# Kernel tuning notes

Hardware: AMD Instinct MI355X
Metric: run time of the kernel (lower is better)

Reference implementation:

```python
import jax, jax.numpy as jnp
import numpy as np

N_NODES = 100000
N_EDGES = 3200000
N_GRAPHS = 256
VOCAB = 1500


def gcn_conv(x, edge_index, W, b, n_nodes):
    # x: [N, Fin], edge_index: [2, E] (row=source, col=target)
    h = x @ W  # [N, Fout]
    loops = jnp.arange(n_nodes, dtype=edge_index.dtype)
    row = jnp.concatenate([edge_index[0], loops])
    col = jnp.concatenate([edge_index[1], loops])
    # symmetric normalization with self-loops (PyG GCNConv default)
    deg = jax.ops.segment_sum(jnp.ones_like(col, dtype=h.dtype), col,
                              num_segments=n_nodes)
    dinv = jnp.where(deg > 0, jax.lax.rsqrt(deg), 0.0)
    norm = dinv[row] * dinv[col]  # [E+N]
    msg = h[row] * norm[:, None]  # gather + scale
    out = jax.ops.segment_sum(msg, col, num_segments=n_nodes)  # scatter-add
    return out + b


def setup_inputs() -> dict:
    key = jax.random.key(0)
    k = jax.random.split(key, 8)
    x_ids = jax.random.randint(k[0], (N_NODES,), 0, VOCAB)
    edge_index = jax.random.randint(k[1], (2, N_EDGES), 0, N_NODES)
    batch = jnp.sort(jax.random.randint(k[2], (N_NODES,), 0, N_GRAPHS))
    emb_table = jax.random.normal(k[3], (VOCAB, 16), dtype=jnp.float32)
    W1 = jax.random.normal(k[4], (16, 32), dtype=jnp.float32) * (1.0 / np.sqrt(16))
    b1 = jnp.zeros((32,), dtype=jnp.float32)
    W2 = jax.random.normal(k[5], (32, 41), dtype=jnp.float32) * (1.0 / np.sqrt(32))
    b2 = jnp.zeros((41,), dtype=jnp.float32)
    return {"x_ids": x_ids, "edge_index": edge_index, "batch": batch,
            "emb_table": emb_table, "W1": W1, "b1": b1, "W2": W2, "b2": b2}


def reference(x_ids, edge_index, batch, emb_table, W1, b1, W2, b2):
    x = emb_table[x_ids]                      # embedding lookup [N,16]
    x = gcn_conv(x, edge_index, W1, b1, N_NODES)
    x = jax.nn.relu(x)                        # dropout is identity in eval
    x = gcn_conv(x, edge_index, W2, b2, N_NODES)
    # scatter_add pooling over graphs in batch
    return jax.ops.segment_sum(x, batch, num_segments=N_GRAPHS)  # [G,41]
```

## Files before the change

### kernel.cpp

```cpp
#include <hip/hip_runtime.h>


constexpr int EPB = 16384;
constexpr int BSH = 8;
constexpr int BKTN = 1 << BSH;
constexpr int CAP = 10240;
constexpr int CAPC = 8704;

__device__ inline unsigned short f2bf(float x) {
  unsigned u = __float_as_uint(x);
  u += 0x7FFF + ((u >> 16) & 1);
  return (unsigned short)(u >> 16);
}
__device__ inline float bf2f(unsigned short h) {
  return __uint_as_float((unsigned)h << 16);
}
__device__ inline unsigned pk(float a, float b) {
  return (unsigned)f2bf(a) | ((unsigned)f2bf(b) << 16);
}
__device__ __forceinline__ void add8(float acc[8], uint4 v) {
  acc[0] += bf2f(v.x & 0xFFFF); acc[1] += bf2f(v.x >> 16);
  acc[2] += bf2f(v.y & 0xFFFF); acc[3] += bf2f(v.y >> 16);
  acc[4] += bf2f(v.z & 0xFFFF); acc[5] += bf2f(v.z >> 16);
  acc[6] += bf2f(v.w & 0xFFFF); acc[7] += bf2f(v.w >> 16);
}

__device__ __forceinline__ void gather8(const unsigned short* __restrict__ base,
                                        const int* list, int st, int dg,
                                        float acc[8]) {
  int j = 0;
  if (dg >= 8) {
    int r0 = list[st], r1 = list[st + 1], r2 = list[st + 2], r3 = list[st + 3];
    uint4 v0 = *(const uint4*)(base + (size_t)r0 * 16);
    uint4 v1 = *(const uint4*)(base + (size_t)r1 * 16);
    uint4 v2 = *(const uint4*)(base + (size_t)r2 * 16);
    uint4 v3 = *(const uint4*)(base + (size_t)r3 * 16);
    for (j = 4; j + 4 <= dg; j += 4) {
      int s0 = list[st + j], s1 = list[st + j + 1];
      int s2 = list[st + j + 2], s3 = list[st + j + 3];
      uint4 w0 = *(const uint4*)(base + (size_t)s0 * 16);
      uint4 w1 = *(const uint4*)(base + (size_t)s1 * 16);
      uint4 w2 = *(const uint4*)(base + (size_t)s2 * 16);
      uint4 w3 = *(const uint4*)(base + (size_t)s3 * 16);
      add8(acc, v0); add8(acc, v1); add8(acc, v2); add8(acc, v3);
      v0 = w0; v1 = w1; v2 = w2; v3 = w3;
    }
    add8(acc, v0); add8(acc, v1); add8(acc, v2); add8(acc, v3);
  }
  for (; j < dg; ++j)
    add8(acc, *(const uint4*)(base + (size_t)list[st + j] * 16));
}

__device__ __forceinline__ void copy_window(int* list, const int* __restrict__ src,
                                            int n, int tid) {
  const int4* s4 = (const int4*)src;
  int4* d4 = (int4*)list;
  int n4 = n >> 2;
  for (int i = tid; i < n4; i += 512) d4[i] = s4[i];
  for (int i = (n4 << 2) + tid; i < n; i += 512) list[i] = src[i];
}

__device__ __forceinline__ int swz(int b, int nblkp) {
  return (b & 7) * (nblkp >> 3) + (b >> 3);
}

__global__ __launch_bounds__(1024) void k_scatter(const int* __restrict__ row,
                                                  const int* __restrict__ col, int E,
                                                  int nbkt, int nblkp,
                                                  int* __restrict__ cursor,
                                                  int* __restrict__ staging) {
  __shared__ int sbuf[EPB];
  __shared__ int cnt[512], sc[512], cur[512], gbase[512];
  int tid = threadIdx.x;
  int lane = tid & 63, wv = tid >> 6;
  int blk = swz(blockIdx.x, nblkp);
  if (tid < 512) cnt[tid] = 0;
  __syncthreads();
  int e0 = blk * EPB, e1 = min(E, e0 + EPB);
  for (int e = e0 + tid; e < e1; e += 1024)
    atomicAdd(&cnt[col[e] >> BSH], 1);
  __syncthreads();
  if (tid < 512) {
    int c = cnt[tid];
    sc[tid] = c;
    gbase[tid] = c ? atomicAdd(&cursor[tid], c) : 0;
  }
  __syncthreads();
  for (int o = 1; o < 512; o <<= 1) {
    int u = (tid < 512 && tid >= o) ? sc[tid - o] : 0;
    __syncthreads();
    if (tid < 512) sc[tid] += u;
    __syncthreads();
  }
  if (tid < 512) { int st = sc[tid] - cnt[tid]; sc[tid] = st; cur[tid] = st; }
  __syncthreads();
  for (int e = e0 + tid; e < e1; e += 1024) {
    int c = col[e];
    int b = c >> BSH;
    int pos = atomicAdd(&cur[b], 1);
    sbuf[pos] = (row[e] << BSH) | (c & (BKTN - 1));
  }
  __syncthreads();
  for (int b = wv; b < nbkt; b += 16) {
    int lbeg = sc[b], lcnt = cnt[b];
    int gb = gbase[b];
    int lim = CAP - gb;
    if (lcnt > lim) lcnt = lim > 0 ? lim : 0;
    int g = b * CAP + gb;
    for (int j = lane; j < lcnt; j += 64)
      staging[g + j] = sbuf[lbeg + j];
  }
}

__global__ __launch_bounds__(512) void k_build(const int* __restrict__ staging,
                                               const int* __restrict__ cursor,
                                               const int* __restrict__ x_ids,
                                               const float* __restrict__ emb,
                                               int N, int nbkt,
                                               int* __restrict__ col_ptr,
                                               int* __restrict__ endp,
                                               float* __restrict__ dinv,
                                               unsigned short* __restrict__ ag1,
                                               int* __restrict__ edge_row) {
  __shared__ int list[CAP];
  __shared__ int cnt[BKTN], sc[BKTN], lcur[BKTN];
  int tid = threadIdx.x, b = blockIdx.x;
  int beg = b * CAP;
  int total = min(cursor[b], CAP);
  int end = beg + total;
  if (tid < BKTN) cnt[tid] = 0;
  __syncthreads();
  for (int i = beg + tid; i < end; i += 512)
    atomicAdd(&cnt[staging[i] & (BKTN - 1)], 1);
  __syncthreads();
  if (tid < BKTN) sc[tid] = cnt[tid];
  __syncthreads();
  for (int o = 1; o < BKTN; o <<= 1) {
    int u = (tid < BKTN && tid >= o) ? sc[tid - o] : 0;
    __syncthreads();
    if (tid < BKTN) sc[tid] += u;
    __syncthreads();
  }
  if (tid < BKTN) {
    int excl = sc[tid] - cnt[tid];
    sc[tid] = excl;
    lcur[tid] = excl;
    int node = (b << BSH) + tid;
    if (node < N) col_ptr[node] = beg + excl;
  }
  if (tid == 0) {
    endp[b] = end;
    if (b == nbkt - 1) col_ptr[N] = end;
  }
  __syncthreads();
  for (int i = beg + tid; i < end; i += 512) {
    int p = staging[i];
    list[atomicAdd(&lcur[p & (BKTN - 1)], 1)] = p >> BSH;
  }
  __syncthreads();
  for (int i = beg + tid; i < end; i += 512)
    edge_row[i] = list[i - beg];
  int nloc = tid >> 1, half = tid & 1;
  int node = (b << BSH) + nloc;
  if (node < N) {
    float d = rsqrtf((float)(cnt[nloc] + 1));
    if (half == 0) dinv[node] = d;
    const float* er = emb + (size_t)x_ids[node] * 16 + half * 8;
    float4 e0 = *(const float4*)(er);
    float4 e1 = *(const float4*)(er + 4);
    uint4 o;
    o.x = pk(e0.x * d, e0.y * d); o.y = pk(e0.z * d, e0.w * d);
    o.z = pk(e1.x * d, e1.y * d); o.w = pk(e1.z * d, e1.w * d);
    *(uint4*)(ag1 + (size_t)node * 16 + half * 8) = o;
  }
}

__global__ __launch_bounds__(512) void k_fuse1(const unsigned short* __restrict__ ag1,
                                               const int* __restrict__ edge_row,
                                               const int* __restrict__ col_ptr,
                                               const int* __restrict__ endp,
                                               const float* __restrict__ dinv,
                                               const float* __restrict__ W1,
                                               const float* __restrict__ b1, int N,
                                               unsigned short* __restrict__ y1g) {
  __shared__ int list[CAPC];
  __shared__ float W[512];
  __shared__ float bb[32];
  int tid = threadIdx.x, b = blockIdx.x;
  W[tid] = W1[tid];
  if (tid < 32) bb[tid] = b1[tid];
  int nloc = tid >> 1, half = tid & 1;
  int node = (b << BSH) + nloc;
  bool valid = node < N;
  int beg = b * CAP;
  int end = endp[b];
  int ms = 0, me = 0;
  float acc[8];
  if (valid) {
    ms = col_ptr[node];
    me = (nloc == BKTN - 1) ? end : col_ptr[node + 1];
    uint4 v = *(const uint4*)(ag1 + (size_t)node * 16 + half * 8);
    acc[0] = bf2f(v.x & 0xFFFF); acc[1] = bf2f(v.x >> 16);
    acc[2] = bf2f(v.y & 0xFFFF); acc[3] = bf2f(v.y >> 16);
    acc[4] = bf2f(v.z & 0xFFFF); acc[5] = bf2f(v.z >> 16);
    acc[6] = bf2f(v.w & 0xFFFF); acc[7] = bf2f(v.w >> 16);
  } else {
#pragma unroll
    for (int k = 0; k < 8; ++k) acc[k] = 0.f;
  }
  for (int cbeg = beg; cbeg < end; cbeg += CAPC) {
    int cend = min(end, cbeg + CAPC);
    __syncthreads();
    copy_window(list, edge_row + cbeg, cend - cbeg, tid);
    __syncthreads();
    if (valid) {
      int st = max(ms, cbeg), en = min(me, cend);
      if (en > st) gather8(ag1 + half * 8, list, st - cbeg, en - st, acc);
    }
  }
  if (!valid) return;
  float d = dinv[node];
  float sx[8], xo[8];
#pragma unroll
  for (int k = 0; k < 8; ++k) sx[k] = acc[k] * d;
#pragma unroll
  for (int k = 0; k < 8; ++k) xo[k] = __shfl_xor(sx[k], 1);
  float x[16];
  if (half == 0) {
#pragma unroll
    for (int k = 0; k < 8; ++k) { x[k] = sx[k]; x[8 + k] = xo[k]; }
  } else {
#pragma unroll
    for (int k = 0; k < 8; ++k) { x[k] = xo[k]; x[8 + k] = sx[k]; }
  }
  int j0 = half * 16;
  float a[16];
#pragma unroll
  for (int j = 0; j < 16; ++j) a[j] = bb[j0 + j];
#pragma unroll
  for (int k = 0; k < 16; ++k) {
    float xv = x[k];
#pragma unroll
    for (int j = 0; j < 16; ++j) a[j] += xv * W[k * 32 + j0 + j];
  }
#pragma unroll
  for (int j = 0; j < 16; ++j) a[j] = fmaxf(a[j], 0.f) * d;
  uint4 o0 = {pk(a[0], a[1]), pk(a[2], a[3]), pk(a[4], a[5]), pk(a[6], a[7])};
  uint4 o1 = {pk(a[8], a[9]), pk(a[10], a[11]), pk(a[12], a[13]), pk(a[14], a[15])};
  unsigned short* yp = y1g + (size_t)half * N * 16 + (size_t)node * 16;
  *(uint4*)(yp) = o0;
  *(uint4*)(yp + 8) = o1;
}

__global__ __launch_bounds__(512) void k_fuse2(const unsigned short* __restrict__ y1g,
                                               const int* __restrict__ edge_row,
                                               const int* __restrict__ col_ptr,
                                               const int* __restrict__ endp,
                                               const float* __restrict__ dinv,
                                               const int* __restrict__ batch, int N,
                                               int nbkt, float* __restrict__ P) {
  __shared__ int list[CAPC];
  __shared__ float pool[8 * 16];
  int bx = blockIdx.x;
  int plane = (bx >> 2) & 1;
  int b = (bx >> 3) * 4 + (bx & 3);
  if (b >= nbkt) return;
  const unsigned short* __restrict__ y1p = y1g + (size_t)plane * N * 16;
  int pofs = plane << 4;
  int tid = threadIdx.x;
  int nloc = tid >> 1, half = tid & 1;
  int node = (b << BSH) + nloc;
  bool valid = node < N;
  int beg = b * CAP;
  int end = endp[b];
  int ms = 0, me = 0;
  float acc[8];
  if (valid) {
    ms = col_ptr[node];
    me = (nloc == BKTN - 1) ? end : col_ptr[node + 1];
    uint4 v = *(const uint4*)(y1p + (size_t)node * 16 + half * 8);
    acc[0] = bf2f(v.x & 0xFFFF); acc[1] = bf2f(v.x >> 16);
    acc[2] = bf2f(v.y & 0xFFFF); acc[3] = bf2f(v.y >> 16);
    acc[4] = bf2f(v.z & 0xFFFF); acc[5] = bf2f(v.z >> 16);
    acc[6] = bf2f(v.w & 0xFFFF); acc[7] = bf2f(v.w >> 16);
  } else {
#pragma unroll
    for (int k = 0; k < 8; ++k) acc[k] = 0.f;
  }
  for (int cbeg = beg; cbeg < end; cbeg += CAPC) {
    int cend = min(end, cbeg + CAPC);
    __syncthreads();
    copy_window(list, edge_row + cbeg, cend - cbeg, tid);
    __syncthreads();
    if (valid) {
      int st = max(ms, cbeg), en = min(me, cend);
      if (en > st) gather8(y1p + half * 8, list, st - cbeg, en - st, acc);
    }
  }
  int myg = -1;
  if (valid) {
    float d = dinv[node];
#pragma unroll
    for (int k = 0; k < 8; ++k) acc[k] *= d;
    myg = batch[node];
  }
  int g0 = batch[b << BSH];
  int g1 = batch[min((b << BSH) + BKTN - 1, N - 1)];
  for (int clo = g0; clo <= g1; clo += 8) {
    for (int j = tid; j < 8 * 16; j += 512) pool[j] = 0.f;
    __syncthreads();
    if (myg >= clo && myg < clo + 8) {
      float* pp = pool + (myg - clo) * 16 + half * 8;
#pragma unroll
      for (int k = 0; k < 8; ++k) atomicAdd(pp + k, acc[k]);
    }
    __syncthreads();
    int ng = min(8, g1 - clo + 1);
    for (int j = tid; j < ng * 16; j += 512)
      atomicAdd(&P[(size_t)(clo + (j >> 4)) * 32 + pofs + (j & 15)], pool[j]);
    __syncthreads();
  }
}

__global__ __launch_bounds__(64) void k_final(const float* __restrict__ P,
                                              const int* __restrict__ batch, int N,
                                              const float* __restrict__ W2,
                                              const float* __restrict__ b2,
                                              float* __restrict__ out) {
  __shared__ float pr[32];
  __shared__ int se[2];
  int g = blockIdx.x, tid = threadIdx.x;
  if (tid < 2) {
    int v = g + tid;
    int lo = 0, hi = N;
    while (lo < hi) {
      int mid = (lo + hi) >> 1;
      if (batch[mid] < v) lo = mid + 1; else hi = mid;
    }
    se[tid] = lo;
  }
  if (tid < 32) pr[tid] = P[(size_t)g * 32 + tid];
  __syncthreads();
  if (tid < 41) {
    float o = (float)(se[1] - se[0]) * b2[tid];
#pragma unroll
    for (int k = 0; k < 32; ++k) o += pr[k] * W2[k * 41 + tid];
    out[(size_t)g * 41 + tid] = o;
  }
}

extern "C" void kernel_launch(void* const* d_in, const int* in_sizes, int n_in,
                              void* d_out, int out_size, void* d_ws, size_t ws_size,
                              hipStream_t stream) {
  const int* x_ids = (const int*)d_in[0];
  const int* edge_index = (const int*)d_in[1];
  const int* batch = (const int*)d_in[2];
  const float* emb = (const float*)d_in[3];
  const float* W1 = (const float*)d_in[4];
  const float* b1 = (const float*)d_in[5];
  const float* W2 = (const float*)d_in[6];
  const float* b2 = (const float*)d_in[7];
  float* out = (float*)d_out;

  const int N = in_sizes[0];
  const int E = in_sizes[1] / 2;
  const int G = out_size / 41;
  const int* row = edge_index;
  const int* col = edge_index + E;

  const int nbkt = (N + BKTN - 1) >> BSH;
  int nblk = (E + EPB - 1) / EPB;
  const int nblkp = (nblk + 7) & ~7;
  const int nbkt4 = (nbkt + 3) & ~3;

  char* ws = (char*)d_ws;
  size_t woff = 0;
  auto alloc = [&](size_t bytes) -> char* {
    char* p = ws + woff;
    woff += (bytes + 255) & ~(size_t)255;
    return p;
  };
  int* staging = (int*)alloc((size_t)nbkt * CAP * 4);
  int* edge_row = (int*)alloc((size_t)nbkt * CAP * 4);
  int* col_ptr = (int*)alloc(((size_t)N + 1) * 4);
  float* dinv = (float*)alloc((size_t)N * 4);
  unsigned short* ag1 = (unsigned short*)alloc((size_t)N * 16 * 2);
  unsigned short* y1g = (unsigned short*)alloc((size_t)N * 32 * 2);
  int* endp = (int*)alloc((size_t)nbkt * 4);
  float* P = (float*)alloc((size_t)G * 32 * 4 + (size_t)nbkt * 4);
  int* cursor = (int*)(P + (size_t)G * 32);
  (void)ws_size; (void)n_in;

  hipMemsetAsync(P, 0, (size_t)G * 32 * 4 + (size_t)nbkt * 4, stream);

  k_scatter<<<nblkp, 1024, 0, stream>>>(row, col, E, nbkt, nblkp, cursor, staging);
  k_build<<<nbkt, 512, 0, stream>>>(staging, cursor, x_ids, emb, N, nbkt,
                                    col_ptr, endp, dinv, ag1, edge_row);
  k_fuse1<<<nbkt, 512, 0, stream>>>(ag1, edge_row, col_ptr, endp, dinv, W1, b1, N, y1g);
  k_fuse2<<<2 * nbkt4, 512, 0, stream>>>(y1g, edge_row, col_ptr, endp, dinv,
                                         batch, N, nbkt, P);
  k_final<<<G, 64, 0, stream>>>(P, batch, N, W2, b2, out);
}
```

Baseline: 209.9 us.

## Split edge lists by source-node half and gather full 32-wide rows in layer two

k_build now sorts each destination bucket's edges into two sub-lists by whether the source node is in the lower or upper half of the node range, producing two CSR offset arrays. k_fuse2 changes from splitting the 32 features into two 16-wide planes to splitting edges by source half. Each block gathers full 32-wide interleaved bf16 rows from one half of y1, so a block's random reads cover half the table and may hit cache better. The cost is a 512-entry scan in k_build, extra offset arrays, a two-pass gather in k_fuse1, and twice as many pooled atomics per block.

After: 219.6 us. 1.05x slower.

```diff
diff --git a/kernel.cpp b/kernel.cpp
--- a/kernel.cpp
+++ b/kernel.cpp
@@ -6,6 +6,7 @@
 constexpr int BKTN = 1 << BSH;
 constexpr int CAP = 10240;
 constexpr int CAPC = 8704;
+constexpr int CAPF = 5376;
 
 __device__ inline unsigned short f2bf(float x) {
   unsigned u = __float_as_uint(x);
@@ -18,7 +19,7 @@
 __device__ inline unsigned pk(float a, float b) {
   return (unsigned)f2bf(a) | ((unsigned)f2bf(b) << 16);
 }
-__device__ __forceinline__ void add8(float acc[8], uint4 v) {
+__device__ __forceinline__ void add8(float* acc, uint4 v) {
   acc[0] += bf2f(v.x & 0xFFFF); acc[1] += bf2f(v.x >> 16);
   acc[2] += bf2f(v.y & 0xFFFF); acc[3] += bf2f(v.y >> 16);
   acc[4] += bf2f(v.z & 0xFFFF); acc[5] += bf2f(v.z >> 16);
@@ -51,6 +52,37 @@
     add8(acc, *(const uint4*)(base + (size_t)list[st + j] * 16));
 }
 
+__device__ __forceinline__ void gather16(const unsigned short* __restrict__ base,
+                                         const int* list, int st, int dg,
+                                         float acc[16]) {
+  int j = 0;
+  if (dg >= 4) {
+    int r0 = list[st], r1 = list[st + 1];
+    uint4 a0 = *(const uint4*)(base + (size_t)r0 * 32);
+    uint4 a1 = *(const uint4*)(base + (size_t)r0 * 32 + 8);
+    uint4 b0 = *(const uint4*)(base + (size_t)r1 * 32);
+    uint4 b1 = *(const uint4*)(base + (size_t)r1 * 32 + 8);
+    for (j = 2; j + 2 <= dg; j += 2) {
+      int s0 = list[st + j], s1 = list[st + j + 1];
+      uint4 c0 = *(const uint4*)(base + (size_t)s0 * 32);
+      uint4 c1 = *(const uint4*)(base + (size_t)s0 * 32 + 8);
+      uint4 d0 = *(const uint4*)(base + (size_t)s1 * 32);
+      uint4 d1 = *(const uint4*)(base + (size_t)s1 * 32 + 8);
+      add8(acc, a0); add8(acc + 8, a1);
+      add8(acc, b0); add8(acc + 8, b1);
+      a0 = c0; a1 = c1; b0 = d0; b1 = d1;
+    }
+    add8(acc, a0); add8(acc + 8, a1);
+    add8(acc, b0); add8(acc + 8, b1);
+  }
+  for (; j < dg; ++j) {
+    int r = list[st + j];
+    uint4 v0 = *(const uint4*)(base + (size_t)r * 32);
+    uint4 v1 = *(const uint4*)(base + (size_t)r * 32 + 8);
+    add8(acc, v0); add8(acc + 8, v1);
+  }
+}
+
 __device__ __forceinline__ void copy_window(int* list, const int* __restrict__ src,
                                             int n, int tid) {
   const int4* s4 = (const int4*)src;
@@ -116,46 +148,48 @@
                                                const int* __restrict__ cursor,
                                                const int* __restrict__ x_ids,
                                                const float* __restrict__ emb,
-                                               int N, int nbkt,
-                                               int* __restrict__ col_ptr,
+                                               int N, int Nh, int nbkt,
+                                               int* __restrict__ cp0,
+                                               int* __restrict__ cp1,
                                                int* __restrict__ endp,
                                                float* __restrict__ dinv,
                                                unsigned short* __restrict__ ag1,
                                                int* __restrict__ edge_row) {
   __shared__ int list[CAP];
-  __shared__ int cnt[BKTN], sc[BKTN], lcur[BKTN];
+  __shared__ int cnt[512], sc[512], lcur[512];
   int tid = threadIdx.x, b = blockIdx.x;
   int beg = b * CAP;
   int total = min(cursor[b], CAP);
   int end = beg + total;
-  if (tid < BKTN) cnt[tid] = 0;
-  __syncthreads();
-  for (int i = beg + tid; i < end; i += 512)
-    atomicAdd(&cnt[staging[i] & (BKTN - 1)], 1);
-  __syncthreads();
-  if (tid < BKTN) sc[tid] = cnt[tid];
-  __syncthreads();
-  for (int o = 1; o < BKTN; o <<= 1) {
-    int u = (tid < BKTN && tid >= o) ? sc[tid - o] : 0;
-    __syncthreads();
-    if (tid < BKTN) sc[tid] += u;
-    __syncthreads();
-  }
-  if (tid < BKTN) {
+  cnt[tid] = 0;
+  __syncthreads();
+  for (int i = beg + tid; i < end; i += 512) {
+    int p = staging[i];
+    int key = ((p >> BSH) >= Nh ? 256 : 0) | (p & (BKTN - 1));
+    atomicAdd(&cnt[key], 1);
+  }
+  __syncthreads();
+  sc[tid] = cnt[tid];
+  __syncthreads();
+  for (int o = 1; o < 512; o <<= 1) {
+    int u = (tid >= o) ? sc[tid - o] : 0;
+    __syncthreads();
+    sc[tid] += u;
+    __syncthreads();
+  }
+  {
     int excl = sc[tid] - cnt[tid];
     sc[tid] = excl;
     lcur[tid] = excl;
-    int node = (b << BSH) + tid;
-    if (node < N) col_ptr[node] = beg + excl;
-  }
-  if (tid == 0) {
-    endp[b] = end;
-    if (b == nbkt - 1) col_ptr[N] = end;
-  }
+    if (tid < 256) cp0[(b << BSH) + tid] = beg + excl;
+    else cp1[(b << BSH) + tid - 256] = beg + excl;
+  }
+  if (tid == 0) endp[b] = end;
   __syncthreads();
   for (int i = beg + tid; i < end; i += 512) {
     int p = staging[i];
-    list[atomicAdd(&lcur[p & (BKTN - 1)], 1)] = p >> BSH;
+    int key = ((p >> BSH) >= Nh ? 256 : 0) | (p & (BKTN - 1));
+    list[atomicAdd(&lcur[key], 1)] = p >> BSH;
   }
   __syncthreads();
   for (int i = beg + tid; i < end; i += 512)
@@ -163,7 +197,8 @@
   int nloc = tid >> 1, half = tid & 1;
   int node = (b << BSH) + nloc;
   if (node < N) {
-    float d = rsqrtf((float)(cnt[nloc] + 1));
+    int deg = cnt[nloc] + cnt[256 + nloc];
+    float d = rsqrtf((float)(deg + 1));
     if (half == 0) dinv[node] = d;
     const float* er = emb + (size_t)x_ids[node] * 16 + half * 8;
     float4 e0 = *(const float4*)(er);
@@ -177,12 +212,13 @@
 
 __global__ __launch_bounds__(512) void k_fuse1(const unsigned short* __restrict__ ag1,
                                                const int* __restrict__ edge_row,
-                                               const int* __restrict__ col_ptr,
+                                               const int* __restrict__ cp0,
+                                               const int* __restrict__ cp1,
                                                const int* __restrict__ endp,
                                                const float* __restrict__ dinv,
                                                const float* __restrict__ W1,
                                                const float* __restrict__ b1, int N,
-                                               unsigned short* __restrict__ y1g) {
+                                               unsigned short* __restrict__ y1) {
   __shared__ int list[CAPC];
   __shared__ float W[512];
   __shared__ float bb[32];
@@ -194,11 +230,14 @@
   bool valid = node < N;
   int beg = b * CAP;
   int end = endp[b];
-  int ms = 0, me = 0;
+  int h1beg = cp1[b << BSH];
+  int s0 = 0, e0 = 0, s1 = 0, e1 = 0;
   float acc[8];
   if (valid) {
-    ms = col_ptr[node];
-    me = (nloc == BKTN - 1) ? end : col_ptr[node + 1];
+    s0 = cp0[node];
+    e0 = (nloc == BKTN - 1) ? h1beg : cp0[node + 1];
+    s1 = cp1[node];
+    e1 = (nloc == BKTN - 1) ? end : cp1[node + 1];
     uint4 v = *(const uint4*)(ag1 + (size_t)node * 16 + half * 8);
     acc[0] = bf2f(v.x & 0xFFFF); acc[1] = bf2f(v.x >> 16);
     acc[2] = bf2f(v.y & 0xFFFF); acc[3] = bf2f(v.y >> 16);
@@ -214,7 +253,9 @@
     copy_window(list, edge_row + cbeg, cend - cbeg, tid);
     __syncthreads();
     if (valid) {
-      int st = max(ms, cbeg), en = min(me, cend);
+      int st = max(s0, cbeg), en = min(e0, cend);
+      if (en > st) gather8(ag1 + half * 8, list, st - cbeg, en - st, acc);
+      st = max(s1, cbeg); en = min(e1, cend);
       if (en > st) gather8(ag1 + half * 8, list, st - cbeg, en - st, acc);
     }
   }
@@ -247,77 +288,88 @@
   for (int j = 0; j < 16; ++j) a[j] = fmaxf(a[j], 0.f) * d;
   uint4 o0 = {pk(a[0], a[1]), pk(a[2], a[3]), pk(a[4], a[5]), pk(a[6], a[7])};
   uint4 o1 = {pk(a[8], a[9]), pk(a[10], a[11]), pk(a[12], a[13]), pk(a[14], a[15])};
-  unsigned short* yp = y1g + (size_t)half * N * 16 + (size_t)node * 16;
+  unsigned short* yp = y1 + (size_t)node * 32 + half * 16;
   *(uint4*)(yp) = o0;
   *(uint4*)(yp + 8) = o1;
 }
 
-__global__ __launch_bounds__(512) void k_fuse2(const unsigned short* __restrict__ y1g,
+__global__ __launch_bounds__(512) void k_fuse2(const unsigned short* __restrict__ y1,
                                                const int* __restrict__ edge_row,
-                                               const int* __restrict__ col_ptr,
+                                               const int* __restrict__ cp0,
+                                               const int* __restrict__ cp1,
                                                const int* __restrict__ endp,
                                                const float* __restrict__ dinv,
-                                               const int* __restrict__ batch, int N,
-                                               int nbkt, float* __restrict__ P) {
-  __shared__ int list[CAPC];
-  __shared__ float pool[8 * 16];
+                                               const int* __restrict__ batch,
+                                               int N, int Nh, int nbkt,
+                                               float* __restrict__ P) {
+  __shared__ int list[CAPF];
+  __shared__ float pool[8 * 32];
   int bx = blockIdx.x;
-  int plane = (bx >> 2) & 1;
+  int hs = (bx >> 2) & 1;
   int b = (bx >> 3) * 4 + (bx & 3);
   if (b >= nbkt) return;
-  const unsigned short* __restrict__ y1p = y1g + (size_t)plane * N * 16;
-  int pofs = plane << 4;
   int tid = threadIdx.x;
   int nloc = tid >> 1, half = tid & 1;
   int node = (b << BSH) + nloc;
   bool valid = node < N;
-  int beg = b * CAP;
   int end = endp[b];
+  int h1beg = cp1[b << BSH];
+  int rbeg = hs ? h1beg : b * CAP;
+  int rend = hs ? end : h1beg;
   int ms = 0, me = 0;
-  float acc[8];
+  float acc[16];
   if (valid) {
-    ms = col_ptr[node];
-    me = (nloc == BKTN - 1) ? end : col_ptr[node + 1];
-    uint4 v = *(const uint4*)(y1p + (size_t)node * 16 + half * 8);
-    acc[0] = bf2f(v.x & 0xFFFF); acc[1] = bf2f(v.x >> 16);
-    acc[2] = bf2f(v.y & 0xFFFF); acc[3] = bf2f(v.y >> 16);
-    acc[4] = bf2f(v.z & 0xFFFF); acc[5] = bf2f(v.z >> 16);
-    acc[6] = bf2f(v.w & 0xFFFF); acc[7] = bf2f(v.w >> 16);
+    if (hs == 0) {
+      ms = cp0[node];
+      me = (nloc == BKTN - 1) ? h1beg : cp0[node + 1];
+    } else {
+      ms = cp1[node];
+      me = (nloc == BKTN - 1) ? end : cp1[node + 1];
+    }
+  }
+  if (valid && ((node >= Nh) ? 1 : 0) == hs) {
+    const unsigned short* sp = y1 + (size_t)node * 32 + half * 16;
+    uint4 v0 = *(const uint4*)(sp);
+    uint4 v1 = *(const uint4*)(sp + 8);
+#pragma unroll
+    for (int k = 0; k < 16; ++k) acc[k] = 0.f;
+    add8(acc, v0); add8(acc + 8, v1);
   } else {
 #pragma unroll
-    for (int k = 0; k < 8; ++k) acc[k] = 0.f;
-  }
-  for (int cbeg = beg; cbeg < end; cbeg += CAPC) {
-    int cend = min(end, cbeg + CAPC);
+    for (int k = 0; k < 16; ++k) acc[k] = 0.f;
+  }
+  for (int cbeg = rbeg; cbeg < rend; cbeg += CAPF) {
+    int cend = min(rend, cbeg + CAPF);
     __syncthreads();
     copy_window(list, edge_row + cbeg, cend - cbeg, tid);
     __syncthreads();
     if (valid) {
       int st = max(ms, cbeg), en = min(me, cend);
-      if (en > st) gather8(y1p + half * 8, list, st - cbeg, en - st, acc);
+      if (en > st) gather16(y1 + half * 16, list, st - cbeg, en - st, acc);
     }
   }
   int myg = -1;
   if (valid) {
     float d = dinv[node];
 #pragma unroll
-    for (int k = 0; k < 8; ++k) acc[k] *= d;
+    for (int k = 0; k < 16; ++k) acc[k] *= d;
     myg = batch[node];
   }
   int g0 = batch[b << BSH];
   int g1 = batch[min((b << BSH) + BKTN - 1, N - 1)];
+  int pofs = half << 4;
   for (int clo = g0; clo <= g1; clo += 8) {
-    for (int j = tid; j < 8 * 16; j += 512) pool[j] = 0.f;
+    for (int j = tid; j < 8 * 32; j += 512) pool[j] = 0.f;
     __syncthreads();
     if (myg >= clo && myg < clo + 8) {
-      float* pp = pool + (myg - clo) * 16 + half * 8;
-#pragma unroll
-      for (int k = 0; k < 8; ++k) atomicAdd(pp + k, acc[k]);
+      float* pp = pool + (myg - clo) * 32 + pofs;
+#pragma unroll
+      for (int k = 0; k < 16; ++k) atomicAdd(pp + k, acc[k]);
     }
     __syncthreads();
     int ng = min(8, g1 - clo + 1);
-    for (int j = tid; j < ng * 16; j += 512)
-      atomicAdd(&P[(size_t)(clo + (j >> 4)) * 32 + pofs + (j & 15)], pool[j]);
+    for (int j = tid; j < ng * 32; j += 512)
+      atomicAdd(&P[(size_t)(clo + (j >> 5)) * 32 + (j & 31)], pool[j]);
     __syncthreads();
   }
 }
@@ -365,6 +417,7 @@
   const int N = in_sizes[0];
   const int E = in_sizes[1] / 2;
   const int G = out_size / 41;
+  const int Nh = N / 2;
   const int* row = edge_index;
   const int* col = edge_index + E;
 
@@ -382,10 +435,11 @@
   };
   int* staging = (int*)alloc((size_t)nbkt * CAP * 4);
   int* edge_row = (int*)alloc((size_t)nbkt * CAP * 4);
-  int* col_ptr = (int*)alloc(((size_t)N + 1) * 4);
+  int* cp0 = (int*)alloc((size_t)nbkt * BKTN * 4);
+  int* cp1 = (int*)alloc((size_t)nbkt * BKTN * 4);
   float* dinv = (float*)alloc((size_t)N * 4);
   unsigned short* ag1 = (unsigned short*)alloc((size_t)N * 16 * 2);
-  unsigned short* y1g = (unsigned short*)alloc((size_t)N * 32 * 2);
+  unsigned short* y1 = (unsigned short*)alloc((size_t)N * 32 * 2);
   int* endp = (int*)alloc((size_t)nbkt * 4);
   float* P = (float*)alloc((size_t)G * 32 * 4 + (size_t)nbkt * 4);
   int* cursor = (int*)(P + (size_t)G * 32);
@@ -394,10 +448,11 @@
   hipMemsetAsync(P, 0, (size_t)G * 32 * 4 + (size_t)nbkt * 4, stream);
 
   k_scatter<<<nblkp, 1024, 0, stream>>>(row, col, E, nbkt, nblkp, cursor, staging);
-  k_build<<<nbkt, 512, 0, stream>>>(staging, cursor, x_ids, emb, N, nbkt,
-                                    col_ptr, endp, dinv, ag1, edge_row);
-  k_fuse1<<<nbkt, 512, 0, stream>>>(ag1, edge_row, col_ptr, endp, dinv, W1, b1, N, y1g);
-  k_fuse2<<<2 * nbkt4, 512, 0, stream>>>(y1g, edge_row, col_ptr, endp, dinv,
-                                         batch, N, nbkt, P);
+  k_build<<<nbkt, 512, 0, stream>>>(staging, cursor, x_ids, emb, N, Nh, nbkt,
+                                    cp0, cp1, endp, dinv, ag1, edge_row);
+  k_fuse1<<<nbkt, 512, 0, stream>>>(ag1, edge_row, cp0, cp1, endp, dinv, W1, b1,
+                                    N, y1);
+  k_fuse2<<<2 * nbkt4, 512, 0, stream>>>(y1, edge_row, cp0, cp1, endp, dinv,
+                                         batch, N, Nh, nbkt, P);
   k_final<<<G, 64, 0, stream>>>(P, batch, N, W2, b2, out);
 }
```

## Interleave layer-1 output rows and split second aggregation by node halves

Applied to the files above, without the earlier changes.

Layer-1 output now goes into one node-major array of 32 bf16 per node instead of two 16-feature planes. The second aggregation kernel gives each block half of a bucket's nodes with all 32 features, using 4 threads per node, rather than all nodes with half the features. Each gathered neighbor row is then one contiguous 64-byte read, and each edge-list window is loaded into shared memory once per node half instead of once per feature plane. Pooling now covers 32 features per graph. In exchange, each thread issues the same number of strided loads, and the plane-based block swizzle is dropped.

After: 202.6 us. 3.5% less time.

```diff
diff --git a/kernel.cpp b/kernel.cpp
--- a/kernel.cpp
+++ b/kernel.cpp
@@ -18,7 +18,7 @@
 __device__ inline unsigned pk(float a, float b) {
   return (unsigned)f2bf(a) | ((unsigned)f2bf(b) << 16);
 }
-__device__ __forceinline__ void add8(float acc[8], uint4 v) {
+__device__ __forceinline__ void add8(float* acc, uint4 v) {
   acc[0] += bf2f(v.x & 0xFFFF); acc[1] += bf2f(v.x >> 16);
   acc[2] += bf2f(v.y & 0xFFFF); acc[3] += bf2f(v.y >> 16);
   acc[4] += bf2f(v.z & 0xFFFF); acc[5] += bf2f(v.z >> 16);
@@ -51,6 +51,32 @@
     add8(acc, *(const uint4*)(base + (size_t)list[st + j] * 16));
 }
 
+__device__ __forceinline__ void gather_quad(const unsigned short* __restrict__ base,
+                                            const int* list, int st, int dg,
+                                            float acc[8]) {
+  int j = 0;
+  if (dg >= 8) {
+    int r0 = list[st], r1 = list[st + 1], r2 = list[st + 2], r3 = list[st + 3];
+    uint4 v0 = *(const uint4*)(base + (size_t)r0 * 32);
+    uint4 v1 = *(const uint4*)(base + (size_t)r1 * 32);
+    uint4 v2 = *(const uint4*)(base + (size_t)r2 * 32);
+    uint4 v3 = *(const uint4*)(base + (size_t)r3 * 32);
+    for (j = 4; j + 4 <= dg; j += 4) {
+      int s0 = list[st + j], s1 = list[st + j + 1];
+      int s2 = list[st + j + 2], s3 = list[st + j + 3];
+      uint4 w0 = *(const uint4*)(base + (size_t)s0 * 32);
+      uint4 w1 = *(const uint4*)(base + (size_t)s1 * 32);
+      uint4 w2 = *(const uint4*)(base + (size_t)s2 * 32);
+      uint4 w3 = *(const uint4*)(base + (size_t)s3 * 32);
+      add8(acc, v0); add8(acc, v1); add8(acc, v2); add8(acc, v3);
+      v0 = w0; v1 = w1; v2 = w2; v3 = w3;
+    }
+    add8(acc, v0); add8(acc, v1); add8(acc, v2); add8(acc, v3);
+  }
+  for (; j < dg; ++j)
+    add8(acc, *(const uint4*)(base + (size_t)list[st + j] * 32));
+}
+
 __device__ __forceinline__ void copy_window(int* list, const int* __restrict__ src,
                                             int n, int tid) {
   const int4* s4 = (const int4*)src;
@@ -182,7 +208,7 @@
                                                const float* __restrict__ dinv,
                                                const float* __restrict__ W1,
                                                const float* __restrict__ b1, int N,
-                                               unsigned short* __restrict__ y1g) {
+                                               unsigned short* __restrict__ y1) {
   __shared__ int list[CAPC];
   __shared__ float W[512];
   __shared__ float bb[32];
@@ -247,38 +273,38 @@
   for (int j = 0; j < 16; ++j) a[j] = fmaxf(a[j], 0.f) * d;
   uint4 o0 = {pk(a[0], a[1]), pk(a[2], a[3]), pk(a[4], a[5]), pk(a[6], a[7])};
   uint4 o1 = {pk(a[8], a[9]), pk(a[10], a[11]), pk(a[12], a[13]), pk(a[14], a[15])};
-  unsigned short* yp = y1g + (size_t)half * N * 16 + (size_t)node * 16;
+  unsigned short* yp = y1 + (size_t)node * 32 + half * 16;
   *(uint4*)(yp) = o0;
   *(uint4*)(yp + 8) = o1;
 }
 
-__global__ __launch_bounds__(512) void k_fuse2(const unsigned short* __restrict__ y1g,
+__global__ __launch_bounds__(512) void k_fuse2(const unsigned short* __restrict__ y1,
                                                const int* __restrict__ edge_row,
                                                const int* __restrict__ col_ptr,
                                                const int* __restrict__ endp,
                                                const float* __restrict__ dinv,
-                                               const int* __restrict__ batch, int N,
-                                               int nbkt, float* __restrict__ P) {
+                                               const int* __restrict__ batch,
+                                               int N, int nbkt,
+                                               float* __restrict__ P) {
   __shared__ int list[CAPC];
-  __shared__ float pool[8 * 16];
+  __shared__ float pool[8 * 32];
   int bx = blockIdx.x;
-  int plane = (bx >> 2) & 1;
-  int b = (bx >> 3) * 4 + (bx & 3);
-  if (b >= nbkt) return;
-  const unsigned short* __restrict__ y1p = y1g + (size_t)plane * N * 16;
-  int pofs = plane << 4;
+  int b = bx >> 1, np = bx & 1;
   int tid = threadIdx.x;
-  int nloc = tid >> 1, half = tid & 1;
+  int nloc = np * 128 + (tid >> 2), qf = tid & 3;
   int node = (b << BSH) + nloc;
   bool valid = node < N;
-  int beg = b * CAP;
   int end = endp[b];
+  int base0 = (b << BSH) + np * 128;
+  int rbeg = col_ptr[min(base0, N)];
+  int rend = (np == 1) ? end : col_ptr[min(base0 + 128, N)];
+  if (base0 >= N) rbeg = rend;
   int ms = 0, me = 0;
   float acc[8];
   if (valid) {
     ms = col_ptr[node];
     me = (nloc == BKTN - 1) ? end : col_ptr[node + 1];
-    uint4 v = *(const uint4*)(y1p + (size_t)node * 16 + half * 8);
+    uint4 v = *(const uint4*)(y1 + (size_t)node * 32 + qf * 8);
     acc[0] = bf2f(v.x & 0xFFFF); acc[1] = bf2f(v.x >> 16);
     acc[2] = bf2f(v.y & 0xFFFF); acc[3] = bf2f(v.y >> 16);
     acc[4] = bf2f(v.z & 0xFFFF); acc[5] = bf2f(v.z >> 16);
@@ -287,14 +313,14 @@
 #pragma unroll
     for (int k = 0; k < 8; ++k) acc[k] = 0.f;
   }
-  for (int cbeg = beg; cbeg < end; cbeg += CAPC) {
-    int cend = min(end, cbeg + CAPC);
+  for (int cbeg = rbeg; cbeg < rend; cbeg += CAPC) {
+    int cend = min(rend, cbeg + CAPC);
     __syncthreads();
     copy_window(list, edge_row + cbeg, cend - cbeg, tid);
     __syncthreads();
     if (valid) {
       int st = max(ms, cbeg), en = min(me, cend);
-      if (en > st) gather8(y1p + half * 8, list, st - cbeg, en - st, acc);
+      if (en > st) gather_quad(y1 + qf * 8, list, st - cbeg, en - st, acc);
     }
   }
   int myg = -1;
@@ -304,20 +330,20 @@
     for (int k = 0; k < 8; ++k) acc[k] *= d;
     myg = batch[node];
   }
-  int g0 = batch[b << BSH];
-  int g1 = batch[min((b << BSH) + BKTN - 1, N - 1)];
+  int g0 = batch[min(base0, N - 1)];
+  int g1 = batch[min(base0 + 127, N - 1)];
   for (int clo = g0; clo <= g1; clo += 8) {
-    for (int j = tid; j < 8 * 16; j += 512) pool[j] = 0.f;
+    for (int j = tid; j < 8 * 32; j += 512) pool[j] = 0.f;
     __syncthreads();
     if (myg >= clo && myg < clo + 8) {
-      float* pp = pool + (myg - clo) * 16 + half * 8;
+      float* pp = pool + (myg - clo) * 32 + qf * 8;
 #pragma unroll
       for (int k = 0; k < 8; ++k) atomicAdd(pp + k, acc[k]);
     }
     __syncthreads();
     int ng = min(8, g1 - clo + 1);
-    for (int j = tid; j < ng * 16; j += 512)
-      atomicAdd(&P[(size_t)(clo + (j >> 4)) * 32 + pofs + (j & 15)], pool[j]);
+    for (int j = tid; j < ng * 32; j += 512)
+      atomicAdd(&P[(size_t)(clo + (j >> 5)) * 32 + (j & 31)], pool[j]);
     __syncthreads();
   }
 }
@@ -371,7 +397,6 @@
   const int nbkt = (N + BKTN - 1) >> BSH;
   int nblk = (E + EPB - 1) / EPB;
   const int nblkp = (nblk + 7) & ~7;
-  const int nbkt4 = (nbkt + 3) & ~3;
 
   char* ws = (char*)d_ws;
   size_t woff = 0;
@@ -385,7 +410,7 @@
   int* col_ptr = (int*)alloc(((size_t)N + 1) * 4);
   float* dinv = (float*)alloc((size_t)N * 4);
   unsigned short* ag1 = (unsigned short*)alloc((size_t)N * 16 * 2);
-  unsigned short* y1g = (unsigned short*)alloc((size_t)N * 32 * 2);
+  unsigned short* y1 = (unsigned short*)alloc((size_t)N * 32 * 2);
   int* endp = (int*)alloc((size_t)nbkt * 4);
   float* P = (float*)alloc((size_t)G * 32 * 4 + (size_t)nbkt * 4);
   int* cursor = (int*)(P + (size_t)G * 32);
@@ -396,8 +421,9 @@
   k_scatter<<<nblkp, 1024, 0, stream>>>(row, col, E, nbkt, nblkp, cursor, staging);
   k_build<<<nbkt, 512, 0, stream>>>(staging, cursor, x_ids, emb, N, nbkt,
                                     col_ptr, endp, dinv, ag1, edge_row);
-  k_fuse1<<<nbkt, 512, 0, stream>>>(ag1, edge_row, col_ptr, endp, dinv, W1, b1, N, y1g);
-  k_fuse2<<<2 * nbkt4, 512, 0, stream>>>(y1g, edge_row, col_ptr, endp, dinv,
-                                         batch, N, nbkt, P);
+  k_fuse1<<<nbkt, 512, 0, stream>>>(ag1, edge_row, col_ptr, endp, dinv, W1, b1,
+                                    N, y1);
+  k_fuse2<<<2 * nbkt, 512, 0, stream>>>(y1, edge_row, col_ptr, endp, dinv,
+                                        batch, N, nbkt, P);
   k_final<<<G, 64, 0, stream>>>(P, batch, N, W2, b2, out);
 }
```
